# Optimization experiments

Hardware: AMD Instinct MI355X
Metric: run time of the kernel (lower is better)

Reference implementation:

```python
import jax, jax.numpy as jnp
import numpy as np

B, S, D = 2, 2048, 2048
H = 16
Q_LORA, KV_LORA = 1536, 512
D_NOPE, D_ROPE, D_V = 128, 64, 128
QK_D = D_NOPE + D_ROPE  # 192
EPS = 1e-6
ROPE_THETA = 10000.0


def rms_norm(x, w, eps=EPS):
    return x * jax.lax.rsqrt(jnp.mean(x * x, axis=-1, keepdims=True) + eps) * w


def apply_rope(x, cos, sin):
    # x: [b, s, h, d]; cos/sin: [s, d//2]; pairs are interleaved (x0,x1),(x2,x3),...
    xr, xi = x[..., 0::2], x[..., 1::2]
    c = cos[None, :, None, :]
    s = sin[None, :, None, :]
    yr = xr * c - xi * s
    yi = xr * s + xi * c
    return jnp.stack([yr, yi], axis=-1).reshape(x.shape)


def setup_inputs() -> dict:
    key = jax.random.key(0)
    ks = jax.random.split(key, 8)
    sd = 0.02
    pos = jnp.arange(S, dtype=jnp.float32)
    inv_freq = 1.0 / (ROPE_THETA ** (jnp.arange(0, D_ROPE, 2, dtype=jnp.float32) / D_ROPE))
    ang = pos[:, None] * inv_freq[None, :]  # [S, D_ROPE//2]
    mask = jnp.triu(jnp.full((S, S), float('-inf'), dtype=jnp.float32), k=1)
    return {
        'x': jax.random.normal(ks[0], (B, S, D), dtype=jnp.float32),
        'freqs_cos': jnp.cos(ang),
        'freqs_sin': jnp.sin(ang),
        'mask': mask,
        'wq_a': jax.random.normal(ks[1], (Q_LORA, D), dtype=jnp.float32) * sd,
        'q_norm_w': jnp.ones((Q_LORA,), dtype=jnp.float32),
        'wq_b': jax.random.normal(ks[2], (H * QK_D, Q_LORA), dtype=jnp.float32) * sd,
        'wkv_a': jax.random.normal(ks[3], (KV_LORA + D_ROPE, D), dtype=jnp.float32) * sd,
        'kv_norm_w': jnp.ones((KV_LORA,), dtype=jnp.float32),
        'wkv_b': jax.random.normal(ks[4], (H * (D_NOPE + D_V), KV_LORA), dtype=jnp.float32) * sd,
        'wo': jax.random.normal(ks[5], (D, H * D_V), dtype=jnp.float32) * sd,
    }


def reference(x, freqs_cos, freqs_sin, mask, wq_a, q_norm_w, wq_b, wkv_a, kv_norm_w, wkv_b, wo):
    b, s, _ = x.shape
    # query path: down-proj -> RMSNorm -> up-proj
    q = rms_norm(x @ wq_a.T, q_norm_w) @ wq_b.T          # [b, s, H*QK_D]
    q = q.reshape(b, s, H, QK_D)
    q_nope, q_pe = q[..., :D_NOPE], q[..., D_NOPE:]
    q_pe = apply_rope(q_pe, freqs_cos, freqs_sin)
    # kv path: joint down-proj, split latent / rope key
    kv_full = x @ wkv_a.T                                 # [b, s, KV_LORA + D_ROPE]
    kv, k_pe = kv_full[..., :KV_LORA], kv_full[..., KV_LORA:]
    k_pe = apply_rope(k_pe[:, :, None, :], freqs_cos, freqs_sin)  # [b, s, 1, D_ROPE]
    q = jnp.concatenate([q_nope, q_pe], axis=-1)          # [b, s, H, QK_D]
    kv = rms_norm(kv, kv_norm_w) @ wkv_b.T                # [b, s, H*(D_NOPE+D_V)]
    kv = kv.reshape(b, s, H, D_NOPE + D_V)
    k_nope, v = kv[..., :D_NOPE], kv[..., D_NOPE:]
    k = jnp.concatenate([k_nope, jnp.broadcast_to(k_pe, (b, s, H, D_ROPE))], axis=-1)
    scale = QK_D ** -0.5
    scores = jnp.einsum('bshd,bthd->bsht', q, k) * scale + mask[None, :, None, :]
    probs = jax.nn.softmax(scores.astype(jnp.float32), axis=-1).astype(x.dtype)
    out = jnp.einsum('bsht,bthd->bshd', probs, v).reshape(b, s, H * D_V)
    return out @ wo.T
```

## Files before the change

kernel.cpp:

```cpp
#include <hip/hip_runtime.h>
#include <hip/hip_bf16.h>

typedef __bf16 bf16_t;
typedef __bf16 bf16x8 __attribute__((ext_vector_type(8)));
typedef __bf16 bf16x4 __attribute__((ext_vector_type(4)));
typedef __bf16 bf16x2 __attribute__((ext_vector_type(2)));
typedef float  f32x4  __attribute__((ext_vector_type(4)));
typedef float  f32x16 __attribute__((ext_vector_type(16)));

#define NB 2
#define NS 2048
#define ND 2048
#define NH 16
#define QLORA 1536
#define KVLORA 512
#define DNOPE 128
#define DROPE 64
#define DVDIM 128
#define QKD 192

#define QSCALE 0.10411754f

#if __has_builtin(__builtin_amdgcn_exp2f)
#define EXP2F(x) __builtin_amdgcn_exp2f(x)
#else
#define EXP2F(x) __expf((x) * 0.69314718056f)
#endif
#if __has_builtin(__builtin_amdgcn_rcpf)
#define RCPF(x) __builtin_amdgcn_rcpf(x)
#else
#define RCPF(x) (1.0f / (x))
#endif

typedef __attribute__((address_space(3))) void as3_void;
typedef __attribute__((address_space(1))) const void as1_void;
__device__ __forceinline__ void gload16(const void* g, void* l) {
  __builtin_amdgcn_global_load_lds((as1_void*)g, (as3_void*)l, 16, 0, 0);
}

__device__ __forceinline__ int pack2(float a, float b) {
  bf16x2 t = {(bf16_t)a, (bf16_t)b};
  return __builtin_bit_cast(int, t);
}

__global__ __launch_bounds__(256) void k_cvt_all(
    const float* __restrict__ x, const float* __restrict__ wqa,
    const float* __restrict__ wqb, const float* __restrict__ wkva,
    const float* __restrict__ wkvb, const float* __restrict__ wo,
    bf16_t* __restrict__ xb, bf16_t* __restrict__ wqab, bf16_t* __restrict__ wqbb,
    bf16_t* __restrict__ wkvab, bf16_t* __restrict__ wkvbb, bf16_t* __restrict__ wob) {
  const int c0 = 2097152, c1 = 2883584, c2 = 4063232, c3 = 4358144, c4 = 4882432,
            c5 = 5931008;
  int i = blockIdx.x * 256 + threadIdx.x;
  for (; i < c5; i += gridDim.x * 256) {
    const float* src;
    bf16_t* dst;
    int off;
    if (i < c0) { src = x; dst = xb; off = i; }
    else if (i < c1) { src = wqa; dst = wqab; off = i - c0; }
    else if (i < c2) { src = wqb; dst = wqbb; off = i - c1; }
    else if (i < c3) { src = wkva; dst = wkvab; off = i - c2; }
    else if (i < c4) { src = wkvb; dst = wkvbb; off = i - c3; }
    else { src = wo; dst = wob; off = i - c4; }
    float4 v = reinterpret_cast<const float4*>(src)[off];
    bf16x4 o = {(bf16_t)v.x, (bf16_t)v.y, (bf16_t)v.z, (bf16_t)v.w};
    reinterpret_cast<bf16x4*>(dst)[off] = o;
  }
}

template <int EPI>
__global__ __launch_bounds__(256) void k_gemm_bt(
    const bf16_t* __restrict__ A, const bf16_t* __restrict__ Bw,
    float* __restrict__ Cf, float* __restrict__ Cf2,
    bf16_t* __restrict__ Kout, bf16_t* __restrict__ Vtout,
    const float* __restrict__ fc, const float* __restrict__ fs,
    int M, int N, int K) {
  __shared__ bf16_t As[2][128 * 64];
  __shared__ bf16_t Bs[2][128 * 64];
  const int tid = threadIdx.x;
  const int lane = tid & 63;
  const int wave = tid >> 6;
  const int wm = (wave >> 1) * 64, wn = (wave & 1) * 64;
  const int m0 = blockIdx.y * 128, n0 = blockIdx.x * 128;
  const int l15 = lane & 15, l4 = lane >> 4;
  const int srow = lane >> 3;
  const int scol = ((lane & 7) ^ srow) * 8;

  const f32x4 Z4 = {0.f, 0.f, 0.f, 0.f};
  f32x4 acc[4][4];
#pragma unroll
  for (int i = 0; i < 4; ++i)
#pragma unroll
    for (int j = 0; j < 4; ++j) acc[i][j] = Z4;

  auto stage = [&](int buf, int k0) {
#pragma unroll
    for (int c = 0; c < 4; ++c) {
      int chunk = c * 4 + wave;
      int row = chunk * 8 + srow;
      gload16(A + (size_t)(m0 + row) * K + k0 + scol, &As[buf][chunk * 512]);
      gload16(Bw + (size_t)(n0 + row) * K + k0 + scol, &Bs[buf][chunk * 512]);
    }
  };

  const int nk = K >> 6;
  stage(0, 0);
  __syncthreads();
  int cur = 0;
#pragma unroll 1
  for (int t = 0; t < nk; ++t) {
    if (t + 1 < nk) stage(cur ^ 1, (t + 1) * 64);
#pragma unroll
    for (int ks = 0; ks < 2; ++ks) {
      int kc = ks * 4 + l4;
      int pc = (kc ^ (l15 & 7)) * 8;
      bf16x8 af[4], bfr[4];
#pragma unroll
      for (int f = 0; f < 4; ++f) {
        af[f] = *reinterpret_cast<const bf16x8*>(&As[cur][(wm + f * 16 + l15) * 64 + pc]);
        bfr[f] = *reinterpret_cast<const bf16x8*>(&Bs[cur][(wn + f * 16 + l15) * 64 + pc]);
      }
#pragma unroll
      for (int fi = 0; fi < 4; ++fi)
#pragma unroll
        for (int fj = 0; fj < 4; ++fj)
          acc[fi][fj] = __builtin_amdgcn_mfma_f32_16x16x32_bf16(af[fi], bfr[fj], acc[fi][fj], 0, 0, 0);
    }
    __syncthreads();
    cur ^= 1;
  }

#pragma unroll
  for (int fi = 0; fi < 4; ++fi) {
#pragma unroll
    for (int fj = 0; fj < 4; ++fj) {
      int col = n0 + wn + fj * 16 + l15;
#pragma unroll
      for (int r = 0; r < 4; ++r) {
        int row = m0 + wm + fi * 16 + l4 * 4 + r;
        float v = acc[fi][fj][r];
        if (EPI == 0) {
          if (col < N) Cf[(size_t)row * N + col] = v;
        } else if (EPI == 1) {
          int h = col >> 8, rr = col & 255;
          int b = row >> 11, s = row & 2047;
          if (rr < DNOPE)
            Kout[(((size_t)(b * NH + h)) * NS + s) * QKD + rr] = (bf16_t)v;
          else
            Vtout[(((size_t)(b * NH + h)) * DVDIM + (rr - DNOPE)) * NS + s] = (bf16_t)v;
        } else if (EPI == 2) {
          int h = col / 192;
          int d = col - h * 192;
          int b = row >> 11, s = row & 2047;
          float y = v;
          if (d >= DNOPE) {
            float pv = __shfl_xor(v, 1);
            int pp = ((d & ~1) - DNOPE) >> 1;
            float c = fc[s * 32 + pp], si = fs[s * 32 + pp];
            y = (col & 1) ? (pv * si + v * c) : (v * c - pv * si);
          }
          Kout[((size_t)(b * NH + h) * NS + s) * QKD + d] = (bf16_t)(y * QSCALE);
        } else {
          if (col < QLORA) Cf[(size_t)row * QLORA + col] = v;
          else if (col < QLORA + KVLORA + DROPE)
            Cf2[(size_t)row * (KVLORA + DROPE) + (col - QLORA)] = v;
        }
      }
    }
  }
}

template <int COLS>
__global__ __launch_bounds__(256) void k_rmsnorm(const float* __restrict__ in,
                                                 const float* __restrict__ w,
                                                 bf16_t* __restrict__ out) {
  int row = blockIdx.x;
  const float* rp = in + (size_t)row * COLS;
  float ss = 0.f;
  for (int c = threadIdx.x * 4; c < COLS; c += 1024) {
    float4 v = *reinterpret_cast<const float4*>(rp + c);
    ss += v.x * v.x + v.y * v.y + v.z * v.z + v.w * v.w;
  }
#pragma unroll
  for (int m = 32; m; m >>= 1) ss += __shfl_xor(ss, m);
  __shared__ float red[4];
  if ((threadIdx.x & 63) == 0) red[threadIdx.x >> 6] = ss;
  __syncthreads();
  float tot = red[0] + red[1] + red[2] + red[3];
  float rs = rsqrtf(tot / (float)COLS + 1e-6f);
  for (int c = threadIdx.x * 4; c < COLS; c += 1024) {
    float4 v = *reinterpret_cast<const float4*>(rp + c);
    bf16x4 o = {(bf16_t)(v.x * rs * w[c]), (bf16_t)(v.y * rs * w[c + 1]),
                (bf16_t)(v.z * rs * w[c + 2]), (bf16_t)(v.w * rs * w[c + 3])};
    *reinterpret_cast<bf16x4*>(out + (size_t)row * COLS + c) = o;
  }
}

__global__ __launch_bounds__(256) void k_kv_post(const float* __restrict__ kvf,
                                                 const float* __restrict__ w,
                                                 const float* __restrict__ fc,
                                                 const float* __restrict__ fs,
                                                 bf16_t* __restrict__ kvn,
                                                 bf16_t* __restrict__ Kb) {
  int row = blockIdx.x;
  const float* rp = kvf + (size_t)row * (KVLORA + DROPE);
  float ss = 0.f;
  float4 v = {0.f, 0.f, 0.f, 0.f};
  if (threadIdx.x < 128) {
    v = reinterpret_cast<const float4*>(rp)[threadIdx.x];
    ss = v.x * v.x + v.y * v.y + v.z * v.z + v.w * v.w;
  }
#pragma unroll
  for (int m = 32; m; m >>= 1) ss += __shfl_xor(ss, m);
  __shared__ float red[4];
  if ((threadIdx.x & 63) == 0) red[threadIdx.x >> 6] = ss;
  __syncthreads();
  float tot = red[0] + red[1] + red[2] + red[3];
  float rs = rsqrtf(tot / (float)KVLORA + 1e-6f);
  if (threadIdx.x < 128) {
    int c = threadIdx.x * 4;
    bf16x4 o = {(bf16_t)(v.x * rs * w[c]), (bf16_t)(v.y * rs * w[c + 1]),
                (bf16_t)(v.z * rs * w[c + 2]), (bf16_t)(v.w * rs * w[c + 3])};
    *reinterpret_cast<bf16x4*>(kvn + (size_t)row * KVLORA + c) = o;
  }
  int b = row >> 11, s = row & 2047;
  if (threadIdx.x < 32) {
    int p = threadIdx.x;
    float x0 = rp[KVLORA + 2 * p], x1 = rp[KVLORA + 2 * p + 1];
    float c = fc[s * 32 + p], si = fs[s * 32 + p];
    float yr = x0 * c - x1 * si, yi = x0 * si + x1 * c;
    bf16_t br = (bf16_t)yr, bi = (bf16_t)yi;
    for (int h = 0; h < NH; ++h) {
      size_t ob = ((size_t)(b * NH + h) * NS + s) * QKD + DNOPE;
      Kb[ob + 2 * p] = br;
      Kb[ob + 2 * p + 1] = bi;
    }
  }
}

__global__ __launch_bounds__(256, 2) void k_attn(const bf16_t* __restrict__ Qb,
                                                 const bf16_t* __restrict__ Kb,
                                                 const bf16_t* __restrict__ Vtb,
                                                 bf16_t* __restrict__ Ao) {
  __shared__ bf16x8 Ks8[2][64 * 24];
  __shared__ bf16x8 Vs8[2][128 * 8];
  const int id = blockIdx.x;
  const int bh = id & 31;
  const int aa = (id >> 5) & 7;
  const int qt = (id >> 8) ? aa : (15 - aa);
  const int b = bh >> 4, h = bh & 15;
  const int tid = threadIdx.x;
  const int lane = tid & 63, wave = tid >> 6;
  const int l31 = lane & 31, hi = lane >> 5;
  const int q0w = qt * 128 + wave * 32;
  const int qg = q0w + l31;
  const int c4 = hi * 4;
  const int ntiles = 2 * qt + 2;
  const size_t bhNS = (size_t)bh * NS;

  const bf16_t* KbB = Kb + bhNS * QKD;
  const bf16_t* VtB = Vtb + (size_t)bh * DVDIM * NS;
  int koff[6], voff[4];
#pragma unroll
  for (int i = 0; i < 6; ++i) {
    int p = tid + i * 256;
    int row = p / 24, pc = p % 24;
    int lc = (pc & ~7) | ((pc ^ row) & 7);
    koff[i] = row * QKD + lc * 8;
  }
#pragma unroll
  for (int i = 0; i < 4; ++i) {
    int p = tid + i * 256;
    int row = p >> 3, pc = p & 7;
    int lc = pc ^ (row & 7);
    voff[i] = row * NS + lc * 8;
  }

  auto stageKV = [&](int buf, int kv0) {
    const bf16_t* ksrc = KbB + kv0 * QKD;
    const bf16_t* vsrc = VtB + kv0;
    bf16x8* kdst = &Ks8[buf][wave * 64];
    bf16x8* vdst = &Vs8[buf][wave * 64];
#pragma unroll
    for (int i = 0; i < 6; ++i) gload16(ksrc + koff[i], kdst + i * 256);
#pragma unroll
    for (int i = 0; i < 4; ++i) gload16(vsrc + voff[i], vdst + i * 256);
  };

  bf16x8 qf[12];
  {
    const bf16_t* qp = Qb + (bhNS + qg) * QKD + hi * 8;
#pragma unroll
    for (int ks = 0; ks < 12; ++ks)
      qf[ks] = *reinterpret_cast<const bf16x8*>(qp + ks * 16);
  }

  f32x16 oacc[4];
#pragma unroll
  for (int d = 0; d < 4; ++d) oacc[d] = {};
  float mrun = -3e38f, lrun = 0.f;

  stageKV(0, 0);
  int cur = 0;

#pragma unroll 1
  for (int kt = 0; kt < ntiles; ++kt) {
    const int kv0 = kt * 64;
    if (kt + 1 < ntiles) {
      stageKV(cur ^ 1, kv0 + 64);
      asm volatile("s_waitcnt vmcnt(10)" ::: "memory");
    } else {
      asm volatile("s_waitcnt vmcnt(0)" ::: "memory");
    }
    __builtin_amdgcn_sched_barrier(0);
    __builtin_amdgcn_s_barrier();
    __builtin_amdgcn_sched_barrier(0);

    if (kv0 <= q0w + 31) {
      f32x16 sacc[2];
      sacc[0] = {};
      sacc[1] = {};
#pragma unroll
      for (int ks = 0; ks < 12; ++ks) {
#pragma unroll
        for (int kh = 0; kh < 2; ++kh) {
          int row = kh * 32 + l31;
          int c = ks * 2 + hi;
          int pc = (c & ~7) | ((c ^ row) & 7);
          sacc[kh] = __builtin_amdgcn_mfma_f32_32x32x16_bf16(Ks8[cur][row * 24 + pc],
                                                             qf[ks], sacc[kh], 0, 0, 0);
        }
      }

      const bool diag = (kv0 + 63 > q0w);
      float mloc = -3e38f;
#pragma unroll
      for (int kh = 0; kh < 2; ++kh)
#pragma unroll
        for (int rg = 0; rg < 16; ++rg) {
          float s = sacc[kh][rg];
          if (diag) {
            int kg = kv0 + kh * 32 + (rg & 3) + 8 * (rg >> 2) + c4;
            if (kg > qg) s = -3e38f;
            sacc[kh][rg] = s;
          }
          mloc = fmaxf(mloc, s);
        }
      mloc = fmaxf(mloc, __shfl_xor(mloc, 32));

      if (!__all(mloc <= mrun)) {
        float mn = fmaxf(mrun, mloc);
        float fac = EXP2F(mrun - mn);
        mrun = mn;
        lrun *= fac;
#pragma unroll
        for (int d = 0; d < 4; ++d)
#pragma unroll
          for (int rg = 0; rg < 16; ++rg) oacc[d][rg] *= fac;
      }

      float rsum = 0.f;
      int W[8][2];
#pragma unroll
      for (int kh = 0; kh < 2; ++kh)
#pragma unroll
        for (int g = 0; g < 4; ++g) {
          float p0 = EXP2F(sacc[kh][4 * g + 0] - mrun);
          float p1 = EXP2F(sacc[kh][4 * g + 1] - mrun);
          float p2 = EXP2F(sacc[kh][4 * g + 2] - mrun);
          float p3 = EXP2F(sacc[kh][4 * g + 3] - mrun);
          rsum += (p0 + p1) + (p2 + p3);
          W[kh * 4 + g][0] = pack2(p0, p1);
          W[kh * 4 + g][1] = pack2(p2, p3);
        }
      rsum += __shfl_xor(rsum, 32);
      lrun += rsum;

      bf16x8 pa[4];
#pragma unroll
      for (int pks = 0; pks < 4; ++pks) {
        int kh = pks >> 1, G0 = (pks & 1) * 2;
        int a0 = W[kh * 4 + G0][0], a1 = W[kh * 4 + G0][1];
        int b0 = W[kh * 4 + G0 + 1][0], b1 = W[kh * 4 + G0 + 1][1];
        int own0 = hi ? b0 : a0, own1 = hi ? b1 : a1;
        int oth0 = hi ? a0 : b0, oth1 = hi ? a1 : b1;
        int rc0 = __shfl_xor(oth0, 32), rc1 = __shfl_xor(oth1, 32);
        int4 wv;
        wv.x = hi ? rc0 : own0;
        wv.y = hi ? rc1 : own1;
        wv.z = hi ? own0 : rc0;
        wv.w = hi ? own1 : rc1;
        pa[pks] = __builtin_bit_cast(bf16x8, wv);
      }

#pragma unroll
      for (int pks = 0; pks < 4; ++pks)
#pragma unroll
        for (int dvt = 0; dvt < 4; ++dvt) {
          int row = dvt * 32 + l31;
          int pc = (pks * 2 + hi) ^ (row & 7);
          oacc[dvt] = __builtin_amdgcn_mfma_f32_32x32x16_bf16(Vs8[cur][row * 8 + pc],
                                                              pa[pks], oacc[dvt], 0, 0, 0);
        }
    }

    __builtin_amdgcn_sched_barrier(0);
    __builtin_amdgcn_s_barrier();
    cur ^= 1;
  }

  float lr = RCPF(lrun);
  bf16_t* base = Ao + ((size_t)(b * NS) + qg) * (NH * DVDIM) + h * DVDIM;
#pragma unroll
  for (int dvt = 0; dvt < 4; ++dvt)
#pragma unroll
    for (int rg4 = 0; rg4 < 4; ++rg4) {
      int dv0 = dvt * 32 + 8 * rg4 + c4;
      bf16x4 o = {(bf16_t)(oacc[dvt][rg4 * 4 + 0] * lr),
                  (bf16_t)(oacc[dvt][rg4 * 4 + 1] * lr),
                  (bf16_t)(oacc[dvt][rg4 * 4 + 2] * lr),
                  (bf16_t)(oacc[dvt][rg4 * 4 + 3] * lr)};
      *reinterpret_cast<bf16x4*>(base + dv0) = o;
    }
}

extern "C" void kernel_launch(void* const* d_in, const int* in_sizes, int n_in,
                              void* d_out, int out_size, void* d_ws, size_t ws_size,
                              hipStream_t stream) {
  (void)in_sizes; (void)n_in; (void)out_size; (void)ws_size;
  const float* x = (const float*)d_in[0];
  const float* fcos = (const float*)d_in[1];
  const float* fsin = (const float*)d_in[2];
  const float* wq_a = (const float*)d_in[4];
  const float* q_norm_w = (const float*)d_in[5];
  const float* wq_b = (const float*)d_in[6];
  const float* wkv_a = (const float*)d_in[7];
  const float* kv_norm_w = (const float*)d_in[8];
  const float* wkv_b = (const float*)d_in[9];
  const float* wo = (const float*)d_in[10];
  float* out = (float*)d_out;

  char* p = (char*)d_ws;
  bf16_t* x_bf = (bf16_t*)(p);
  bf16_t* wqa_bf = (bf16_t*)(p + 16777216);
  bf16_t* wkva_bf = (bf16_t*)(p + 23068672);
  bf16_t* wqb_bf = (bf16_t*)(p + 25427968);
  bf16_t* wkvb_bf = (bf16_t*)(p + 34865152);
  bf16_t* wo_bf = (bf16_t*)(p + 39059456);
  float* qa_f32 = (float*)(p + 47448064);
  bf16_t* Kb = (bf16_t*)(p + 47448064);
  bf16_t* qan_bf = (bf16_t*)(p + 72613888);
  bf16_t* Qb = (bf16_t*)(p + 85196800);
  char* r2 = p + 110362624;
  float* kvf_f32 = (float*)(r2);
  bf16_t* kvn_bf = (bf16_t*)(r2 + 9437184);
  bf16_t* Vtb = (bf16_t*)(r2 + 13631488);
  bf16_t* attn_bf = (bf16_t*)(r2 + 30408704);

  k_cvt_all<<<2048, 256, 0, stream>>>(x, wq_a, wq_b, wkv_a, wkv_b, wo, x_bf, wqa_bf,
                                      wqb_bf, wkva_bf, wkvb_bf, wo_bf);

  k_gemm_bt<3><<<dim3(17, 32), 256, 0, stream>>>(x_bf, wqa_bf, qa_f32, kvf_f32,
                                                 nullptr, nullptr, nullptr, nullptr,
                                                 NB * NS, QLORA + KVLORA + DROPE, ND);
  k_rmsnorm<QLORA><<<NB * NS, 256, 0, stream>>>(qa_f32, q_norm_w, qan_bf);
  k_kv_post<<<NB * NS, 256, 0, stream>>>(kvf_f32, kv_norm_w, fcos, fsin, kvn_bf, Kb);
  k_gemm_bt<2><<<dim3(24, 32), 256, 0, stream>>>(qan_bf, wqb_bf, nullptr, nullptr, Qb,
                                                 nullptr, fcos, fsin, NB * NS, NH * QKD,
                                                 QLORA);
  k_gemm_bt<1><<<dim3(32, 32), 256, 0, stream>>>(kvn_bf, wkvb_bf, nullptr, nullptr, Kb,
                                                 Vtb, nullptr, nullptr, NB * NS,
                                                 NH * (DNOPE + DVDIM), KVLORA);
  k_attn<<<dim3(512), 256, 0, stream>>>(Qb, Kb, Vtb, attn_bf);
  k_gemm_bt<0><<<dim3(16, 32), 256, 0, stream>>>(attn_bf, wo_bf, out, nullptr, nullptr,
                                                 nullptr, nullptr, nullptr, NB * NS, ND,
                                                 NH * DVDIM);
}
```

Measured before the change: 366.5 us.

## Shrink GEMM tile to 128x64 and drop LDS double buffering

Changes the shared GEMM kernel from 128x128 tiles with a double-buffered LDS prefetch to 128x64 tiles with a single buffer, where each wave owns 32 rows across all 64 columns. Grids are doubled in the N dimension, giving more blocks to fill the GPU's compute units and using less LDS per block, which may allow higher occupancy. The cost is lost overlap between global loads and MFMA work, an extra barrier per k-step, and lower arithmetic intensity per tile. Bounds checks on columns are removed because the N sizes now divide evenly by 64.

```diff
diff --git a/kernel.cpp b/kernel.cpp
--- a/kernel.cpp
+++ b/kernel.cpp
@@ -75,72 +75,71 @@
     bf16_t* __restrict__ Kout, bf16_t* __restrict__ Vtout,
     const float* __restrict__ fc, const float* __restrict__ fs,
     int M, int N, int K) {
-  __shared__ bf16_t As[2][128 * 64];
-  __shared__ bf16_t Bs[2][128 * 64];
+  __shared__ bf16_t As[128 * 64];
+  __shared__ bf16_t Bs[64 * 64];
   const int tid = threadIdx.x;
   const int lane = tid & 63;
   const int wave = tid >> 6;
-  const int wm = (wave >> 1) * 64, wn = (wave & 1) * 64;
-  const int m0 = blockIdx.y * 128, n0 = blockIdx.x * 128;
+  const int m0 = blockIdx.y * 128, n0 = blockIdx.x * 64;
   const int l15 = lane & 15, l4 = lane >> 4;
   const int srow = lane >> 3;
   const int scol = ((lane & 7) ^ srow) * 8;
 
   const f32x4 Z4 = {0.f, 0.f, 0.f, 0.f};
-  f32x4 acc[4][4];
-#pragma unroll
-  for (int i = 0; i < 4; ++i)
+  f32x4 acc[2][4];
+#pragma unroll
+  for (int i = 0; i < 2; ++i)
 #pragma unroll
     for (int j = 0; j < 4; ++j) acc[i][j] = Z4;
 
-  auto stage = [&](int buf, int k0) {
+  const int nk = K >> 6;
+#pragma unroll 1
+  for (int t = 0; t < nk; ++t) {
+    const int k0 = t * 64;
+    __syncthreads();
 #pragma unroll
     for (int c = 0; c < 4; ++c) {
       int chunk = c * 4 + wave;
       int row = chunk * 8 + srow;
-      gload16(A + (size_t)(m0 + row) * K + k0 + scol, &As[buf][chunk * 512]);
-      gload16(Bw + (size_t)(n0 + row) * K + k0 + scol, &Bs[buf][chunk * 512]);
-    }
-  };
-
-  const int nk = K >> 6;
-  stage(0, 0);
-  __syncthreads();
-  int cur = 0;
-#pragma unroll 1
-  for (int t = 0; t < nk; ++t) {
-    if (t + 1 < nk) stage(cur ^ 1, (t + 1) * 64);
+      gload16(A + (size_t)(m0 + row) * K + k0 + scol, &As[chunk * 512]);
+    }
+#pragma unroll
+    for (int c = 0; c < 2; ++c) {
+      int chunk = c * 4 + wave;
+      int row = chunk * 8 + srow;
+      gload16(Bw + (size_t)(n0 + row) * K + k0 + scol, &Bs[chunk * 512]);
+    }
+    __syncthreads();
 #pragma unroll
     for (int ks = 0; ks < 2; ++ks) {
       int kc = ks * 4 + l4;
       int pc = (kc ^ (l15 & 7)) * 8;
-      bf16x8 af[4], bfr[4];
-#pragma unroll
-      for (int f = 0; f < 4; ++f) {
-        af[f] = *reinterpret_cast<const bf16x8*>(&As[cur][(wm + f * 16 + l15) * 64 + pc]);
-        bfr[f] = *reinterpret_cast<const bf16x8*>(&Bs[cur][(wn + f * 16 + l15) * 64 + pc]);
-      }
-#pragma unroll
-      for (int fi = 0; fi < 4; ++fi)
+      bf16x8 af[2], bfr[4];
+#pragma unroll
+      for (int f = 0; f < 2; ++f)
+        af[f] = *reinterpret_cast<const bf16x8*>(&As[(wave * 32 + f * 16 + l15) * 64 + pc]);
+#pragma unroll
+      for (int f = 0; f < 4; ++f)
+        bfr[f] = *reinterpret_cast<const bf16x8*>(&Bs[(f * 16 + l15) * 64 + pc]);
+#pragma unroll
+      for (int fi = 0; fi < 2; ++fi)
 #pragma unroll
         for (int fj = 0; fj < 4; ++fj)
           acc[fi][fj] = __builtin_amdgcn_mfma_f32_16x16x32_bf16(af[fi], bfr[fj], acc[fi][fj], 0, 0, 0);
     }
-    __syncthreads();
-    cur ^= 1;
-  }
-
-#pragma unroll
-  for (int fi = 0; fi < 4; ++fi) {
+  }
+
+#pragma unroll
+  for (int fi = 0; fi < 2; ++fi) {
 #pragma unroll
     for (int fj = 0; fj < 4; ++fj) {
-      int col = n0 + wn + fj * 16 + l15;
+      int col = n0 + fj * 16 + l15;
 #pragma unroll
       for (int r = 0; r < 4; ++r) {
-        int row = m0 + wm + fi * 16 + l4 * 4 + r;
+        int row = m0 + wave * 32 + fi * 16 + l4 * 4 + r;
         float v = acc[fi][fj][r];
         if (EPI == 0) {
-          if (col < N) Cf[(size_t)row * N + col] = v;
+          Cf[(size_t)row * N + col] = v;
         } else if (EPI == 1) {
           int h = col >> 8, rr = col & 255;
           int b = row >> 11, s = row & 2047;
@@ -162,8 +161,7 @@
           Kout[((size_t)(b * NH + h) * NS + s) * QKD + d] = (bf16_t)(y * QSCALE);
         } else {
           if (col < QLORA) Cf[(size_t)row * QLORA + col] = v;
-          else if (col < QLORA + KVLORA + DROPE)
-            Cf2[(size_t)row * (KVLORA + DROPE) + (col - QLORA)] = v;
+          else Cf2[(size_t)row * (KVLORA + DROPE) + (col - QLORA)] = v;
         }
       }
     }
@@ -460,19 +458,19 @@
   k_cvt_all<<<2048, 256, 0, stream>>>(x, wq_a, wq_b, wkv_a, wkv_b, wo, x_bf, wqa_bf,
                                       wqb_bf, wkva_bf, wkvb_bf, wo_bf);
 
-  k_gemm_bt<3><<<dim3(17, 32), 256, 0, stream>>>(x_bf, wqa_bf, qa_f32, kvf_f32,
+  k_gemm_bt<3><<<dim3(33, 32), 256, 0, stream>>>(x_bf, wqa_bf, qa_f32, kvf_f32,
                                                  nullptr, nullptr, nullptr, nullptr,
                                                  NB * NS, QLORA + KVLORA + DROPE, ND);
   k_rmsnorm<QLORA><<<NB * NS, 256, 0, stream>>>(qa_f32, q_norm_w, qan_bf);
   k_kv_post<<<NB * NS, 256, 0, stream>>>(kvf_f32, kv_norm_w, fcos, fsin, kvn_bf, Kb);
-  k_gemm_bt<2><<<dim3(24, 32), 256, 0, stream>>>(qan_bf, wqb_bf, nullptr, nullptr, Qb,
+  k_gemm_bt<2><<<dim3(48, 32), 256, 0, stream>>>(qan_bf, wqb_bf, nullptr, nullptr, Qb,
                                                  nullptr, fcos, fsin, NB * NS, NH * QKD,
                                                  QLORA);
-  k_gemm_bt<1><<<dim3(32, 32), 256, 0, stream>>>(kvn_bf, wkvb_bf, nullptr, nullptr, Kb,
+  k_gemm_bt<1><<<dim3(64, 32), 256, 0, stream>>>(kvn_bf, wkvb_bf, nullptr, nullptr, Kb,
                                                  Vtb, nullptr, nullptr, NB * NS,
                                                  NH * (DNOPE + DVDIM), KVLORA);
   k_attn<<<dim3(512), 256, 0, stream>>>(Qb, Kb, Vtb, attn_bf);
-  k_gemm_bt<0><<<dim3(16, 32), 256, 0, stream>>>(attn_bf, wo_bf, out, nullptr, nullptr,
+  k_gemm_bt<0><<<dim3(32, 32), 256, 0, stream>>>(attn_bf, wo_bf, out, nullptr, nullptr,
                                                  nullptr, nullptr, nullptr, NB * NS, ND,
                                                  NH * DVDIM);
 }
```

New measurement: 365.8 us. About the same (-0.2%).
